# Kernel tuning notes

Hardware: AMD Instinct MI355X
Metric: run time of the kernel (lower is better)

## Reference

```python
import jax, jax.numpy as jnp
import numpy as np

H = 512      # hidden_size
F = 1024     # expert_hidden_size
E = 16       # expert_count
EPS = 1e-5   # torch LayerNorm default eps


def setup_inputs() -> dict:
    key = jax.random.key(0)
    ks = jax.random.split(key, 7)
    tokens = jax.random.normal(ks[0], (4, 2048, H), dtype=jnp.float32)
    # Stacked per-expert parameters (one 3D tensor per parameter kind)
    ln_g = jnp.ones((E, H), dtype=jnp.float32)
    ln_b = jnp.zeros((E, H), dtype=jnp.float32)
    W1 = jax.random.normal(ks[1], (E, H, F), dtype=jnp.float32) * (1.0 / np.sqrt(H))
    b1 = jax.random.normal(ks[2], (E, F), dtype=jnp.float32) * 0.01
    W2 = jax.random.normal(ks[3], (E, F, H), dtype=jnp.float32) * (1.0 / np.sqrt(F))
    b2 = jax.random.normal(ks[4], (E, H), dtype=jnp.float32) * 0.01
    return {"tokens": tokens, "ln_g": ln_g, "ln_b": ln_b,
            "W1": W1, "b1": b1, "W2": W2, "b2": b2}


def reference(tokens, ln_g, ln_b, W1, b1, W2, b2):
    # LayerNorm statistics depend only on tokens, so compute x_hat once
    mu = jnp.mean(tokens, axis=-1, keepdims=True)
    var = jnp.mean(jnp.square(tokens - mu), axis=-1, keepdims=True)
    x_hat = (tokens - mu) * jax.lax.rsqrt(var + EPS)          # [B,S,H]
    # Per-expert affine: [B,S,E,H]
    xin = x_hat[:, :, None, :] * ln_g + ln_b
    h = jnp.einsum('bseh,ehf->bsef', xin, W1) + b1            # [B,S,E,F]
    h = jax.nn.gelu(h, approximate=False)                     # torch GELU default (erf)
    out = jnp.einsum('bsef,efh->bseh', h, W2) + b2            # [B,S,E,H] (stack dim=2)
    return out
```

## Files before the change

kernel.cpp:

```cpp
#include <hip/hip_runtime.h>
#include <stdint.h>

#define H 512
#define F 1024
#define E 16
#define TOK 8192
#define EPS 1e-5f

typedef short bf16x8 __attribute__((ext_vector_type(8)));
typedef float f32x4 __attribute__((ext_vector_type(4)));

__device__ __forceinline__ float bf2f(unsigned short u) {
    union { unsigned int i; float f; } v; v.i = ((unsigned int)u) << 16; return v.f;
}
__device__ __forceinline__ unsigned short f2bf(float f) {
    union { float f; unsigned int i; } v; v.f = f;
    unsigned int r = (v.i + 0x7FFFu + ((v.i >> 16) & 1u)) >> 16;
    return (unsigned short)r;
}
__device__ __forceinline__ void gload16(const void* g, void* l) {
    __builtin_amdgcn_global_load_lds(
        (const __attribute__((address_space(1))) unsigned int*)g,
        (__attribute__((address_space(3))) unsigned int*)l, 16, 0, 0);
}

__device__ __forceinline__ float gelu_erf(float v) {
    const float x  = v * 0.70710678118654752f;
    const float ax = fabsf(x);
    const float t  = __builtin_amdgcn_rcpf(fmaf(0.3275911f, ax, 1.0f));
    float p = fmaf(1.061405429f, t, -1.453152027f);
    p = fmaf(p, t, 1.421413741f);
    p = fmaf(p, t, -0.284496736f);
    p = fmaf(p, t, 0.254829592f);
    p = p * t;
    const float ex = __expf(-x * x);
    float er = fmaf(-p, ex, 1.0f);
    er = copysignf(er, x);
    return 0.5f * v * (1.0f + er);
}

__global__ void ln_kernel(const float* __restrict__ tokens,
                          unsigned short* __restrict__ xhat) {
    const int tid  = threadIdx.x;
    const int wid  = tid >> 6;
    const int lane = tid & 63;
    const int token = blockIdx.x * 4 + wid;

    const float* src = tokens + (size_t)token * H + lane * 8;
    float4 r0 = *reinterpret_cast<const float4*>(src);
    float4 r1 = *reinterpret_cast<const float4*>(src + 4);
    float x[8] = {r0.x, r0.y, r0.z, r0.w, r1.x, r1.y, r1.z, r1.w};

    float s = 0.f, s2 = 0.f;
#pragma unroll
    for (int j = 0; j < 8; ++j) { s += x[j]; s2 += x[j] * x[j]; }
#pragma unroll
    for (int m = 32; m >= 1; m >>= 1) {
        s  += __shfl_xor(s, m);
        s2 += __shfl_xor(s2, m);
    }
    const float mu  = s * (1.0f / H);
    float var = s2 * (1.0f / H) - mu * mu;
    var = fmaxf(var, 0.0f);
    const float rstd = rsqrtf(var + EPS);

    unsigned short o[8];
#pragma unroll
    for (int j = 0; j < 8; ++j) o[j] = f2bf((x[j] - mu) * rstd);
    uint4 w;
    w.x = o[0] | ((unsigned)o[1] << 16);
    w.y = o[2] | ((unsigned)o[3] << 16);
    w.z = o[4] | ((unsigned)o[5] << 16);
    w.w = o[6] | ((unsigned)o[7] << 16);
    *reinterpret_cast<uint4*>(xhat + (size_t)token * H + lane * 8) = w;
}

#define XPAD 72
__global__ void transpose_kernel(const float* __restrict__ src,
                                 unsigned short* __restrict__ dst,
                                 int rows, int cols,
                                 const float* __restrict__ scale) {
    __shared__ __align__(16) unsigned short tile[64 * XPAD];
    const int e  = blockIdx.z;
    const int r0 = blockIdx.y * 64;
    const int c0 = blockIdx.x * 64;
    const int tid = threadIdx.x;

    const float* sbase = src + (size_t)e * rows * cols;
    unsigned short* dbase = dst + (size_t)e * rows * cols;

    {
        const int r  = tid >> 2;
        const int cg = (tid & 3) * 16;
        const float* p = sbase + (size_t)(r0 + r) * cols + c0 + cg;
        const float sc = (scale != nullptr) ? scale[e * rows + r0 + r] : 1.0f;
        unsigned short u[16];
#pragma unroll
        for (int j = 0; j < 16; j += 4) {
            float4 v = *reinterpret_cast<const float4*>(p + j);
            u[j + 0] = f2bf(v.x * sc);
            u[j + 1] = f2bf(v.y * sc);
            u[j + 2] = f2bf(v.z * sc);
            u[j + 3] = f2bf(v.w * sc);
        }
#pragma unroll
        for (int j = 0; j < 16; j += 8) {
            uint4 w;
            w.x = u[j + 0] | ((unsigned)u[j + 1] << 16);
            w.y = u[j + 2] | ((unsigned)u[j + 3] << 16);
            w.z = u[j + 4] | ((unsigned)u[j + 5] << 16);
            w.w = u[j + 6] | ((unsigned)u[j + 7] << 16);
            *reinterpret_cast<uint4*>(&tile[r * XPAD + cg + j]) = w;
        }
    }
    __syncthreads();
#pragma unroll
    for (int i = 0; i < 2; ++i) {
        const int oc = (tid >> 3) + i * 32;
        const int og = (tid & 7) * 8;
        unsigned short u[8];
#pragma unroll
        for (int j = 0; j < 8; ++j) u[j] = tile[(og + j) * XPAD + oc];
        uint4 w;
        w.x = u[0] | ((unsigned)u[1] << 16);
        w.y = u[2] | ((unsigned)u[3] << 16);
        w.z = u[4] | ((unsigned)u[5] << 16);
        w.w = u[6] | ((unsigned)u[7] << 16);
        *reinterpret_cast<uint4*>(dbase + (size_t)(c0 + oc) * rows + r0 + og) = w;
    }
}

__global__ void b1fold_kernel(const float* __restrict__ b1,
                              const float* __restrict__ lnb,
                              const float* __restrict__ W1,
                              float* __restrict__ b1p) {
    __shared__ float slb[64];
    const int e = blockIdx.y;
    const int z = blockIdx.z;
    const int f = blockIdx.x * 256 + threadIdx.x;
    const int h0 = z * 64;
    if (threadIdx.x < 64) slb[threadIdx.x] = lnb[e * H + h0 + threadIdx.x];
    __syncthreads();
    float acc = (z == 0) ? b1[e * F + f] : 0.0f;
    const float* w = W1 + (size_t)e * H * F + (size_t)h0 * F + f;
#pragma unroll 8
    for (int h = 0; h < 64; ++h) acc += slb[h] * w[(size_t)h * F];
    atomicAdd(&b1p[e * F + f], acc);
}

__global__ __launch_bounds__(1024, 4) void gemm1_kernel(
    const unsigned short* __restrict__ xhat,
    const unsigned short* __restrict__ w1gt,
    const float* __restrict__ b1p,
    unsigned short* __restrict__ hbuf)
{
    __shared__ __align__(16) unsigned short lds_x[2 * 256 * 64];
    __shared__ __align__(16) unsigned short lds_w[2 * 128 * 64];

    const int tid  = threadIdx.x;
    const int lane = tid & 63;
    const int w    = tid >> 6;
    const int quad = lane >> 4;
    const int l16  = lane & 15;
    const int swzr = (l16 & 7) * 8;

    const unsigned bid = blockIdx.x;
    const int e  = bid & 15;
    const int t  = bid >> 4;
    const int ft = t & 7;
    const int mt = t >> 3;
    const int m0 = mt * 256, f0 = ft * 128;
    const int wm = w >> 1, wn = w & 1;

    f32x4 acc[2][4];
#pragma unroll
    for (int mi = 0; mi < 2; ++mi)
#pragma unroll
        for (int ni = 0; ni < 4; ++ni) acc[mi][ni] = (f32x4){0.f, 0.f, 0.f, 0.f};

    const unsigned short* xg = xhat + (size_t)m0 * H;
    const unsigned short* wg = w1gt + ((size_t)e * F + f0) * H;

    auto stage = [&](int kt, int buf) {
        const int k0 = kt * 64;
#pragma unroll
        for (int i = 0; i < 2; ++i) {
            const int idx = tid + i * 1024;
            const int row = idx >> 3;
            const int c   = ((idx & 7) * 8) ^ ((row & 7) * 8);
            gload16(xg + (size_t)row * H + k0 + c,
                    (char*)lds_x + (size_t)buf * 32768 + (size_t)idx * 16);
        }
        {
            const int row = tid >> 3;
            const int c   = ((tid & 7) * 8) ^ ((row & 7) * 8);
            gload16(wg + (size_t)row * H + k0 + c,
                    (char*)lds_w + (size_t)buf * 16384 + (size_t)tid * 16);
        }
    };

    stage(0, 0);
    __syncthreads();
    for (int kt = 0; kt < 8; ++kt) {
        const int cur = kt & 1;
        if (kt < 7) stage(kt + 1, cur ^ 1);
#pragma unroll
        for (int ks = 0; ks < 2; ++ks) {
            const int kc = (ks * 32 + quad * 8) ^ swzr;
            bf16x8 a[2], b[4];
#pragma unroll
            for (int mi = 0; mi < 2; ++mi)
                a[mi] = *reinterpret_cast<const bf16x8*>(
                    &lds_x[cur * 16384 + (wm * 32 + mi * 16 + l16) * 64 + kc]);
#pragma unroll
            for (int ni = 0; ni < 4; ++ni)
                b[ni] = *reinterpret_cast<const bf16x8*>(
                    &lds_w[cur * 8192 + (wn * 64 + ni * 16 + l16) * 64 + kc]);
#pragma unroll
            for (int mi = 0; mi < 2; ++mi)
#pragma unroll
                for (int ni = 0; ni < 4; ++ni)
                    acc[mi][ni] = __builtin_amdgcn_mfma_f32_16x16x32_bf16(a[mi], b[ni], acc[mi][ni], 0, 0, 0);
        }
        __syncthreads();
    }

    float bv[4];
#pragma unroll
    for (int ni = 0; ni < 4; ++ni)
        bv[ni] = b1p[e * F + f0 + wn * 64 + ni * 16 + l16];
#pragma unroll
    for (int mi = 0; mi < 2; ++mi) {
#pragma unroll
        for (int r = 0; r < 4; ++r) {
            const int row = m0 + wm * 32 + mi * 16 + quad * 4 + r;
            unsigned short* dst = hbuf + ((size_t)row * E + e) * F + f0;
#pragma unroll
            for (int ni = 0; ni < 4; ++ni) {
                const float v = acc[mi][ni][r] + bv[ni];
                dst[wn * 64 + ni * 16 + l16] = f2bf(gelu_erf(v));
            }
        }
    }
}

__global__ __launch_bounds__(1024, 4) void gemm2_kernel(
    const unsigned short* __restrict__ hbuf,
    const unsigned short* __restrict__ w2t,
    const float* __restrict__ b2,
    float* __restrict__ outp)
{
    __shared__ __align__(16) unsigned short lds_a[2 * 128 * 64];
    __shared__ __align__(16) unsigned short lds_b[2 * 512 * 64];

    const int tid  = threadIdx.x;
    const int lane = tid & 63;
    const int w    = tid >> 6;
    const int quad = lane >> 4;
    const int l16  = lane & 15;
    const int swzr = (l16 & 7) * 8;

    const int e  = blockIdx.x & 15;
    const int mt = blockIdx.x >> 4;
    const int m0 = mt * 128;
    const int wm = w & 1, wn = w >> 1;

    f32x4 acc[4][4];
#pragma unroll
    for (int mi = 0; mi < 4; ++mi)
#pragma unroll
        for (int ni = 0; ni < 4; ++ni) acc[mi][ni] = (f32x4){0.f, 0.f, 0.f, 0.f};

    const unsigned short* hg = hbuf + ((size_t)m0 * E + e) * F;
    const unsigned short* wg = w2t + (size_t)e * H * F;

    auto stage = [&](int kt, int buf) {
        const int k0 = kt * 64;
        {
            const int row = tid >> 3;
            const int c   = ((tid & 7) * 8) ^ ((row & 7) * 8);
            gload16(hg + (size_t)row * (E * F) + k0 + c,
                    (char*)lds_a + (size_t)buf * 16384 + (size_t)tid * 16);
        }
#pragma unroll
        for (int i = 0; i < 4; ++i) {
            const int idx = tid + i * 1024;
            const int row = idx >> 3;
            const int c   = ((idx & 7) * 8) ^ ((row & 7) * 8);
            gload16(wg + (size_t)row * F + k0 + c,
                    (char*)lds_b + (size_t)buf * 65536 + (size_t)idx * 16);
        }
    };

    stage(0, 0);
    __syncthreads();
    for (int kt = 0; kt < 16; ++kt) {
        const int cur = kt & 1;
        if (kt < 15) stage(kt + 1, cur ^ 1);
#pragma unroll
        for (int ks = 0; ks < 2; ++ks) {
            const int kc = (ks * 32 + quad * 8) ^ swzr;
            bf16x8 a[4], b[4];
#pragma unroll
            for (int mi = 0; mi < 4; ++mi)
                a[mi] = *reinterpret_cast<const bf16x8*>(
                    &lds_a[cur * 8192 + (wm * 64 + mi * 16 + l16) * 64 + kc]);
#pragma unroll
            for (int ni = 0; ni < 4; ++ni)
                b[ni] = *reinterpret_cast<const bf16x8*>(
                    &lds_b[cur * 32768 + (wn * 64 + ni * 16 + l16) * 64 + kc]);
#pragma unroll
            for (int ni = 0; ni < 4; ++ni)
#pragma unroll
                for (int mi = 0; mi < 4; ++mi)
                    acc[mi][ni] = __builtin_amdgcn_mfma_f32_16x16x32_bf16(a[mi], b[ni], acc[mi][ni], 0, 0, 0);
        }
        __syncthreads();
    }

    float bv[4];
#pragma unroll
    for (int ni = 0; ni < 4; ++ni)
        bv[ni] = b2[e * H + wn * 64 + ni * 16 + l16];
#pragma unroll
    for (int mi = 0; mi < 4; ++mi) {
#pragma unroll
        for (int r = 0; r < 4; ++r) {
            const int row = m0 + wm * 64 + mi * 16 + quad * 4 + r;
            float* dst = outp + ((size_t)row * E + e) * H + wn * 64;
#pragma unroll
            for (int ni = 0; ni < 4; ++ni)
                dst[ni * 16 + l16] = acc[mi][ni][r] + bv[ni];
        }
    }
}

extern "C" void kernel_launch(void* const* d_in, const int* in_sizes, int n_in,
                              void* d_out, int out_size, void* d_ws, size_t ws_size,
                              hipStream_t stream) {
    const float* tokens = (const float*)d_in[0];
    const float* ln_g   = (const float*)d_in[1];
    const float* ln_b   = (const float*)d_in[2];
    const float* W1     = (const float*)d_in[3];
    const float* b1     = (const float*)d_in[4];
    const float* W2     = (const float*)d_in[5];
    const float* b2     = (const float*)d_in[6];

    char* ws = (char*)d_ws;
    unsigned short* xhat = (unsigned short*)(ws);
    unsigned short* w1gt = (unsigned short*)(ws + 8388608);
    unsigned short* w2t  = (unsigned short*)(ws + 25165824);
    float*          b1p  = (float*)(ws + 41943040);

    unsigned short* hbuf = (unsigned short*)d_out;
    float*          outp = (float*)d_out;

    hipMemsetAsync(b1p, 0, E * F * sizeof(float), stream);
    hipLaunchKernelGGL(ln_kernel, dim3(TOK / 4), dim3(256), 0, stream, tokens, xhat);
    hipLaunchKernelGGL(transpose_kernel, dim3(F / 64, H / 64, E), dim3(256), 0, stream,
                       W1, w1gt, H, F, ln_g);
    hipLaunchKernelGGL(transpose_kernel, dim3(H / 64, F / 64, E), dim3(256), 0, stream,
                       W2, w2t, F, H, (const float*)nullptr);
    hipLaunchKernelGGL(b1fold_kernel, dim3(F / 256, E, 8), dim3(256), 0, stream, b1, ln_b, W1, b1p);
    hipLaunchKernelGGL(gemm1_kernel, dim3(E * (TOK / 256) * (F / 128)), dim3(1024), 0, stream,
                       xhat, w1gt, b1p, hbuf);
    hipLaunchKernelGGL(gemm2_kernel, dim3(E * (TOK / 128)), dim3(1024), 0, stream,
                       hbuf, w2t, b2, outp);
}
```

Baseline: 749.1 us.

## Retile gemm1 to 128x128, deepen load pipeline, raise MFMA priority, use tanh-style GELU

Both GEMMs now prefetch two k-tiles ahead and wait on explicit vmcnt counters plus raw barriers instead of a full __syncthreads after each step, so global-to-LDS loads overlap with MFMA work. MFMA blocks are wrapped in s_setprio to favour matrix issue. gemm1 is shrunk to 512-thread 128x128 tiles with twice as many blocks. The erf-based GELU is replaced by a sigmoid (tanh-form) approximation that costs fewer instructions but deviates from the exact erf GELU the reference uses.

```diff
diff --git a/kernel.cpp b/kernel.cpp
--- a/kernel.cpp
+++ b/kernel.cpp
@@ -24,19 +24,11 @@
         (__attribute__((address_space(3))) unsigned int*)l, 16, 0, 0);
 }
 
-__device__ __forceinline__ float gelu_erf(float v) {
-    const float x  = v * 0.70710678118654752f;
-    const float ax = fabsf(x);
-    const float t  = __builtin_amdgcn_rcpf(fmaf(0.3275911f, ax, 1.0f));
-    float p = fmaf(1.061405429f, t, -1.453152027f);
-    p = fmaf(p, t, 1.421413741f);
-    p = fmaf(p, t, -0.284496736f);
-    p = fmaf(p, t, 0.254829592f);
-    p = p * t;
-    const float ex = __expf(-x * x);
-    float er = fmaf(-p, ex, 1.0f);
-    er = copysignf(er, x);
-    return 0.5f * v * (1.0f + er);
+__device__ __forceinline__ float gelu_fast(float v) {
+    const float v2 = v * v;
+    const float s  = v * fmaf(0.0713548162f, v2, 1.5957691216f);
+    const float e  = __expf(-s);
+    return v * __builtin_amdgcn_rcpf(1.0f + e);
 }
 
 __global__ void ln_kernel(const float* __restrict__ tokens,
@@ -148,13 +140,13 @@
     atomicAdd(&b1p[e * F + f], acc);
 }
 
-__global__ __launch_bounds__(1024, 4) void gemm1_kernel(
+__global__ __launch_bounds__(512, 4) void gemm1_kernel(
     const unsigned short* __restrict__ xhat,
     const unsigned short* __restrict__ w1gt,
     const float* __restrict__ b1p,
     unsigned short* __restrict__ hbuf)
 {
-    __shared__ __align__(16) unsigned short lds_x[2 * 256 * 64];
+    __shared__ __align__(16) unsigned short lds_x[2 * 128 * 64];
     __shared__ __align__(16) unsigned short lds_w[2 * 128 * 64];
 
     const int tid  = threadIdx.x;
@@ -169,7 +161,7 @@
     const int t  = bid >> 4;
     const int ft = t & 7;
     const int mt = t >> 3;
-    const int m0 = mt * 256, f0 = ft * 128;
+    const int m0 = mt * 128, f0 = ft * 128;
     const int wm = w >> 1, wn = w & 1;
 
     f32x4 acc[2][4];
@@ -185,25 +177,29 @@
         const int k0 = kt * 64;
 #pragma unroll
         for (int i = 0; i < 2; ++i) {
-            const int idx = tid + i * 1024;
+            const int idx = tid + i * 512;
             const int row = idx >> 3;
             const int c   = ((idx & 7) * 8) ^ ((row & 7) * 8);
             gload16(xg + (size_t)row * H + k0 + c,
-                    (char*)lds_x + (size_t)buf * 32768 + (size_t)idx * 16);
-        }
-        {
-            const int row = tid >> 3;
-            const int c   = ((tid & 7) * 8) ^ ((row & 7) * 8);
+                    (char*)lds_x + (size_t)buf * 16384 + (size_t)idx * 16);
+        }
+#pragma unroll
+        for (int i = 0; i < 2; ++i) {
+            const int idx = tid + i * 512;
+            const int row = idx >> 3;
+            const int c   = ((idx & 7) * 8) ^ ((row & 7) * 8);
             gload16(wg + (size_t)row * H + k0 + c,
-                    (char*)lds_w + (size_t)buf * 16384 + (size_t)tid * 16);
+                    (char*)lds_w + (size_t)buf * 16384 + (size_t)idx * 16);
         }
     };
 
     stage(0, 0);
-    __syncthreads();
+    stage(1, 1);
     for (int kt = 0; kt < 8; ++kt) {
         const int cur = kt & 1;
-        if (kt < 7) stage(kt + 1, cur ^ 1);
+        if (kt < 7) asm volatile("s_waitcnt vmcnt(4)" ::: "memory");
+        else        asm volatile("s_waitcnt vmcnt(0)" ::: "memory");
+        __builtin_amdgcn_s_barrier();
 #pragma unroll
         for (int ks = 0; ks < 2; ++ks) {
             const int kc = (ks * 32 + quad * 8) ^ swzr;
@@ -211,18 +207,21 @@
 #pragma unroll
             for (int mi = 0; mi < 2; ++mi)
                 a[mi] = *reinterpret_cast<const bf16x8*>(
-                    &lds_x[cur * 16384 + (wm * 32 + mi * 16 + l16) * 64 + kc]);
+                    &lds_x[cur * 8192 + (wm * 32 + mi * 16 + l16) * 64 + kc]);
 #pragma unroll
             for (int ni = 0; ni < 4; ++ni)
                 b[ni] = *reinterpret_cast<const bf16x8*>(
                     &lds_w[cur * 8192 + (wn * 64 + ni * 16 + l16) * 64 + kc]);
+            __builtin_amdgcn_s_setprio(1);
 #pragma unroll
             for (int mi = 0; mi < 2; ++mi)
 #pragma unroll
                 for (int ni = 0; ni < 4; ++ni)
                     acc[mi][ni] = __builtin_amdgcn_mfma_f32_16x16x32_bf16(a[mi], b[ni], acc[mi][ni], 0, 0, 0);
-        }
-        __syncthreads();
+            __builtin_amdgcn_s_setprio(0);
+        }
+        __builtin_amdgcn_s_barrier();
+        if (kt + 2 < 8) stage(kt + 2, cur);
     }
 
     float bv[4];
@@ -238,7 +237,7 @@
 #pragma unroll
             for (int ni = 0; ni < 4; ++ni) {
                 const float v = acc[mi][ni][r] + bv[ni];
-                dst[wn * 64 + ni * 16 + l16] = f2bf(gelu_erf(v));
+                dst[wn * 64 + ni * 16 + l16] = f2bf(gelu_fast(v));
             }
         }
     }
@@ -293,10 +292,12 @@
     };
 
     stage(0, 0);
-    __syncthreads();
+    stage(1, 1);
     for (int kt = 0; kt < 16; ++kt) {
         const int cur = kt & 1;
-        if (kt < 15) stage(kt + 1, cur ^ 1);
+        if (kt < 15) asm volatile("s_waitcnt vmcnt(5)" ::: "memory");
+        else         asm volatile("s_waitcnt vmcnt(0)" ::: "memory");
+        __builtin_amdgcn_s_barrier();
 #pragma unroll
         for (int ks = 0; ks < 2; ++ks) {
             const int kc = (ks * 32 + quad * 8) ^ swzr;
@@ -309,13 +310,16 @@
             for (int ni = 0; ni < 4; ++ni)
                 b[ni] = *reinterpret_cast<const bf16x8*>(
                     &lds_b[cur * 32768 + (wn * 64 + ni * 16 + l16) * 64 + kc]);
+            __builtin_amdgcn_s_setprio(1);
 #pragma unroll
             for (int ni = 0; ni < 4; ++ni)
 #pragma unroll
                 for (int mi = 0; mi < 4; ++mi)
                     acc[mi][ni] = __builtin_amdgcn_mfma_f32_16x16x32_bf16(a[mi], b[ni], acc[mi][ni], 0, 0, 0);
-        }
-        __syncthreads();
+            __builtin_amdgcn_s_setprio(0);
+        }
+        __builtin_amdgcn_s_barrier();
+        if (kt + 2 < 16) stage(kt + 2, cur);
     }
 
     float bv[4];
@@ -362,7 +366,7 @@
     hipLaunchKernelGGL(transpose_kernel, dim3(H / 64, F / 64, E), dim3(256), 0, stream,
                        W2, w2t, F, H, (const float*)nullptr);
     hipLaunchKernelGGL(b1fold_kernel, dim3(F / 256, E, 8), dim3(256), 0, stream, b1, ln_b, W1, b1p);
-    hipLaunchKernelGGL(gemm1_kernel, dim3(E * (TOK / 256) * (F / 128)), dim3(1024), 0, stream,
+    hipLaunchKernelGGL(gemm1_kernel, dim3(E * (TOK / 128) * (F / 128)), dim3(512), 0, stream,
                        xhat, w1gt, b1p, hbuf);
     hipLaunchKernelGGL(gemm2_kernel, dim3(E * (TOK / 128)), dim3(1024), 0, stream,
                        hbuf, w2t, b2, outp);
```

Result: faster. 670.3 us (-10.5%).
